# Kernel tuning notes

Measured on AMD Instinct MI355X. Metric: run time of the kernel, lower is better.

Reference implementation:

```python
import jax, jax.numpy as jnp
import numpy as np

N_NODES = 10000
N_EDGES = 640000
D_IN, D_HID, D_OUT = 128, 256, 64


def setup_inputs() -> dict:
    key = jax.random.key(0)
    k = jax.random.split(key, 8)
    h = jax.random.normal(k[0], (N_NODES, D_IN), dtype=jnp.float32)
    w = jax.random.uniform(k[1], (N_EDGES, 1), dtype=jnp.float32)
    src = jax.random.randint(k[2], (N_EDGES,), 0, N_NODES, dtype=jnp.int32)
    dst = jax.random.randint(k[3], (N_EDGES,), 0, N_NODES, dtype=jnp.int32)
    W1 = jax.random.normal(k[4], (2 * D_IN, D_HID), dtype=jnp.float32) * (1.0 / np.sqrt(2 * D_IN))
    b1 = jnp.zeros((D_HID,), dtype=jnp.float32)
    W2 = jax.random.normal(k[5], (2 * D_HID, D_OUT), dtype=jnp.float32) * (1.0 / np.sqrt(2 * D_HID))
    b2 = jnp.zeros((D_OUT,), dtype=jnp.float32)
    return {"h": h, "w": w, "src": src, "dst": dst, "W1": W1, "b1": b1, "W2": W2, "b2": b2}


def _sage_layer(h, w, src, dst, W, b, n_nodes):
    # message: m_e = h[src_e] * w_e  (scalar edge weight broadcast over features)
    m = h[src] * w  # [E, D]
    # mean scatter-reduce over incoming edges per destination node
    s = jax.ops.segment_sum(m, dst, num_segments=n_nodes)          # [N, D]
    deg = jax.ops.segment_sum(jnp.ones((dst.shape[0],), h.dtype), dst, num_segments=n_nodes)
    h_N = jnp.where(deg[:, None] > 0, s / jnp.maximum(deg, 1.0)[:, None], 0.0)
    # concat + linear
    return jnp.concatenate([h, h_N], axis=1) @ W + b


def reference(h, w, src, dst, W1, b1, W2, b2):
    n = h.shape[0]
    x = _sage_layer(h, w, src, dst, W1, b1, n)
    x = jax.nn.relu(x)
    return _sage_layer(x, w, src, dst, W2, b2, n)
```

## Files before the change

### kernel.cpp

```cpp
#include <hip/hip_runtime.h>
#include <hip/hip_fp16.h>


#define CAPS 64

typedef _Float16 f16x8 __attribute__((ext_vector_type(8)));
typedef float f32x4 __attribute__((ext_vector_type(4)));


__global__ void fill_k(const int* __restrict__ src, const int* __restrict__ dst,
                       const float* __restrict__ w, int* __restrict__ cursor,
                       unsigned int* __restrict__ ebuf, int E) {
  int i = blockIdx.x * blockDim.x + threadIdx.x;
  if (i < E) {
    const int d = dst[i];
    const int sub = i & 3;
    const int p = atomicAdd(&cursor[d * 4 + sub], 1);
    if (p < CAPS) {
      const __half hw = __float2half_rn(w[i]);
      ebuf[((size_t)(d * 4 + sub)) * CAPS + p] =
          ((unsigned int)src[i] << 16) | (unsigned int)__half_as_ushort(hw);
    }
  }
}

__global__ void cast_h_k(const float* __restrict__ h, __half* __restrict__ hh, int n4) {
  int i = blockIdx.x * blockDim.x + threadIdx.x;
  if (i < n4) {
    float4 v = reinterpret_cast<const float4*>(h)[i];
    reinterpret_cast<__half2*>(hh)[2 * i] = __floats2half2_rn(v.x, v.y);
    reinterpret_cast<__half2*>(hh)[2 * i + 1] = __floats2half2_rn(v.z, v.w);
  }
}

__global__ void w1swz_k(const float* __restrict__ W1, __half* __restrict__ Bz) {
  const int t = blockIdx.x * blockDim.x + threadIdx.x;
  if (t >= 8192) return;
  const int lane = t & 63;
  const int nt = (t >> 6) & 15;
  const int kc = t >> 10;
  const int kbase = kc * 32 + (lane >> 4) * 8;
  const int n = nt * 16 + (lane & 15);
  __half tmp[8];
#pragma unroll
  for (int j = 0; j < 8; ++j)
    tmp[j] = __float2half_rn(W1[(size_t)(kbase + j) * 256 + n]);
  *reinterpret_cast<uint4*>(Bz + (size_t)t * 8) = *reinterpret_cast<uint4*>(tmp);
}

__global__ void w2swz_k(const float* __restrict__ W2, __half* __restrict__ Bz) {
  const int t = blockIdx.x * blockDim.x + threadIdx.x;
  if (t >= 4096) return;
  const int lane = t & 63;
  const int nt = (t >> 6) & 7;
  const int kc = t >> 9;
  const int kbase = kc * 32 + (lane >> 4) * 8;
  const int np = nt * 16 + (lane & 15);
  __half tmp[8];
#pragma unroll
  for (int j = 0; j < 8; ++j) {
    const int k = kbase + j;
    const float v = (np < 64) ? W2[(size_t)k * 64 + np]
                              : W2[(size_t)(256 + k) * 64 + (np - 64)];
    tmp[j] = __float2half_rn(v);
  }
  *reinterpret_cast<uint4*>(Bz + (size_t)t * 8) = *reinterpret_cast<uint4*>(tmp);
}


__global__ __launch_bounds__(256) void agg1_k(const __half* __restrict__ hh,
                                              const unsigned int* __restrict__ ebuf,
                                              const int* __restrict__ cnt,
                                              __half* __restrict__ G1, int N) {
  const int n = blockIdx.x * 4 + (threadIdx.x >> 6);
  if (n >= N) return;
  const int lane = threadIdx.x & 63;
  const int g = lane >> 5;
  const int f = lane & 31;
  const uint2* __restrict__ H = reinterpret_cast<const uint2*>(hh);
  float a0 = 0.f, a1 = 0.f, a2 = 0.f, a3 = 0.f;
  int deg = 0;
#pragma unroll
  for (int seg = 0; seg < 4; ++seg) {
    const int m = min(cnt[n * 4 + seg], CAPS);
    deg += m;
    const unsigned int* __restrict__ bkt = ebuf + ((size_t)(n * 4 + seg)) * CAPS;
    const unsigned int pk = (lane < m) ? bkt[lane] : 0u;
    int j = 0;
    for (; j + 3 < m; j += 4) {
      const unsigned int pA = __shfl(pk, j + g);
      const unsigned int pB = __shfl(pk, j + 2 + g);
      const int eA = (int)(pA >> 16), eB = (int)(pB >> 16);
      const float wA = __half2float(__ushort_as_half((unsigned short)pA));
      const float wB = __half2float(__ushort_as_half((unsigned short)pB));
      const uint2 qA = H[(size_t)eA * 32 + f];
      const uint2 qB = H[(size_t)eB * 32 + f];
      const float2 fA0 = __half22float2(*(const __half2*)&qA.x);
      const float2 fA1 = __half22float2(*(const __half2*)&qA.y);
      const float2 fB0 = __half22float2(*(const __half2*)&qB.x);
      const float2 fB1 = __half22float2(*(const __half2*)&qB.y);
      a0 += fA0.x * wA + fB0.x * wB;
      a1 += fA0.y * wA + fB0.y * wB;
      a2 += fA1.x * wA + fB1.x * wB;
      a3 += fA1.y * wA + fB1.y * wB;
    }
    for (; j < m; j += 2) {
      const int jj = j + g;
      const unsigned int p = __shfl(pk, jj < m ? jj : (m - 1));
      const int e = (int)(p >> 16);
      float wt = __half2float(__ushort_as_half((unsigned short)p));
      if (jj >= m) wt = 0.f;
      const uint2 q = H[(size_t)e * 32 + f];
      const float2 f0 = __half22float2(*(const __half2*)&q.x);
      const float2 f1 = __half22float2(*(const __half2*)&q.y);
      a0 += f0.x * wt;
      a1 += f0.y * wt;
      a2 += f1.x * wt;
      a3 += f1.y * wt;
    }
  }
  a0 += __shfl_xor(a0, 32);
  a1 += __shfl_xor(a1, 32);
  a2 += __shfl_xor(a2, 32);
  a3 += __shfl_xor(a3, 32);
  if (lane < 32) {
    const float inv = (deg > 0) ? 1.0f / (float)deg : 0.0f;
    const __half2 p01 = __floats2half2_rn(a0 * inv, a1 * inv);
    const __half2 p23 = __floats2half2_rn(a2 * inv, a3 * inv);
    uint2 q;
    q.x = *reinterpret_cast<const unsigned int*>(&p01);
    q.y = *reinterpret_cast<const unsigned int*>(&p23);
    reinterpret_cast<uint2*>(G1)[(size_t)n * 32 + lane] = q;
  }
}


__global__ __launch_bounds__(256) void gemm1_k(const __half* __restrict__ hh,
                                               const __half* __restrict__ G1,
                                               const __half* __restrict__ Bz,
                                               const float* __restrict__ bias,
                                               __half* __restrict__ H1) {
  const int tid = threadIdx.x;
  const int w = tid >> 6, lane = tid & 63;
  const int m0 = blockIdx.x * 16;
  const int row_in = m0 + (lane & 15);
  const int qoff = (lane >> 4) * 8;
  f32x4 acc[4] = {};
  const __half* __restrict__ Ah = hh + (size_t)row_in * 128;
  const __half* __restrict__ Ag = G1 + (size_t)row_in * 128;
#pragma unroll
  for (int kc = 0; kc < 8; ++kc) {
    const __half* asrc = (kc < 4) ? (Ah + kc * 32 + qoff) : (Ag + (kc - 4) * 32 + qoff);
    const f16x8 af = *reinterpret_cast<const f16x8*>(asrc);
    const __half* bbase = Bz + ((size_t)(kc * 16 + w * 4) * 64 + lane) * 8;
#pragma unroll
    for (int nt = 0; nt < 4; ++nt) {
      const f16x8 bf = *reinterpret_cast<const f16x8*>(bbase + (size_t)nt * 64 * 8);
      acc[nt] = __builtin_amdgcn_mfma_f32_16x16x32_f16(af, bf, acc[nt], 0, 0, 0);
    }
  }
  __shared__ __half Hs[16][264];
  const int colq = lane & 15;
  const int rowq = (lane >> 4) * 4;
#pragma unroll
  for (int nt = 0; nt < 4; ++nt) {
    const int col = w * 64 + nt * 16 + colq;
    const float bz = bias[col];
#pragma unroll
    for (int r = 0; r < 4; ++r)
      Hs[rowq + r][col] = __float2half_rn(fmaxf(acc[nt][r] + bz, 0.f));
  }
  __syncthreads();
  const int r8 = tid >> 5;
  const int c32 = tid & 31;
#pragma unroll
  for (int it = 0; it < 2; ++it) {
    const int row = it * 8 + r8;
    const uint4 q = *reinterpret_cast<const uint4*>(&Hs[row][c32 * 8]);
    *reinterpret_cast<uint4*>(&H1[((size_t)(m0 + row)) * 256 + c32 * 8]) = q;
  }
}


__global__ __launch_bounds__(256) void gemmZU_k(const __half* __restrict__ H1,
                                                const __half* __restrict__ Bz,
                                                __half* __restrict__ Z,
                                                float* __restrict__ U, int M) {
  const int tid = threadIdx.x;
  const int w = tid >> 6, lane = tid & 63;
  const int m0 = blockIdx.x * 32;
  const int mh = w >> 1, nh = w & 1;
  const int row_in = m0 + mh * 16 + (lane & 15);
  const int qoff = (lane >> 4) * 8;
  f32x4 acc[4] = {};
  const __half* __restrict__ Ar = H1 + (size_t)row_in * 256;
#pragma unroll
  for (int kc = 0; kc < 8; ++kc) {
    const f16x8 af = *reinterpret_cast<const f16x8*>(Ar + kc * 32 + qoff);
    const __half* bbase = Bz + ((size_t)(kc * 8 + nh * 4) * 64 + lane) * 8;
#pragma unroll
    for (int nt = 0; nt < 4; ++nt) {
      const f16x8 bf = *reinterpret_cast<const f16x8*>(bbase + (size_t)nt * 64 * 8);
      acc[nt] = __builtin_amdgcn_mfma_f32_16x16x32_f16(af, bf, acc[nt], 0, 0, 0);
    }
  }
  __shared__ float S[32][132];
  const int colq = lane & 15;
  const int rowq = (lane >> 4) * 4;
#pragma unroll
  for (int nt = 0; nt < 4; ++nt) {
    const int col = nh * 64 + nt * 16 + colq;
#pragma unroll
    for (int r = 0; r < 4; ++r) S[mh * 16 + rowq + r][col] = acc[nt][r];
  }
  __syncthreads();
#pragma unroll
  for (int it = 0; it < 2; ++it) {
    const int idx = it * 256 + tid;
    const int row = idx >> 4, c4 = idx & 15;
    const int grow = m0 + row;
    if (grow < M) {
      const float4 v = make_float4(S[row][c4 * 4], S[row][c4 * 4 + 1],
                                   S[row][c4 * 4 + 2], S[row][c4 * 4 + 3]);
      *reinterpret_cast<float4*>(&U[(size_t)grow * 64 + c4 * 4]) = v;
    }
  }
  {
    const int row = tid >> 3, c8 = tid & 7;
    const int grow = m0 + row;
    if (grow < M) {
      const float* s = &S[row][64 + c8 * 8];
      const __half2 h0 = __floats2half2_rn(s[0], s[1]);
      const __half2 h1 = __floats2half2_rn(s[2], s[3]);
      const __half2 h2 = __floats2half2_rn(s[4], s[5]);
      const __half2 h3 = __floats2half2_rn(s[6], s[7]);
      uint4 q;
      q.x = *reinterpret_cast<const unsigned int*>(&h0);
      q.y = *reinterpret_cast<const unsigned int*>(&h1);
      q.z = *reinterpret_cast<const unsigned int*>(&h2);
      q.w = *reinterpret_cast<const unsigned int*>(&h3);
      *reinterpret_cast<uint4*>(&Z[(size_t)grow * 64 + c8 * 8]) = q;
    }
  }
}


__global__ __launch_bounds__(256) void agg2z_k(const __half* __restrict__ Z,
                                               const float* __restrict__ U,
                                               const float* __restrict__ b2,
                                               const unsigned int* __restrict__ ebuf,
                                               const int* __restrict__ cnt,
                                               float* __restrict__ out, int N) {
  const int n = blockIdx.x * 4 + (threadIdx.x >> 6);
  if (n >= N) return;
  const int lane = threadIdx.x & 63;
  const int g = lane >> 4;
  const int f = lane & 15;
  const uint2* __restrict__ Zr = reinterpret_cast<const uint2*>(Z);
  float a0 = 0.f, a1 = 0.f, a2 = 0.f, a3 = 0.f;
  int deg = 0;
#pragma unroll
  for (int seg = 0; seg < 4; ++seg) {
    const int m = min(cnt[n * 4 + seg], CAPS);
    deg += m;
    const unsigned int* __restrict__ bkt = ebuf + ((size_t)(n * 4 + seg)) * CAPS;
    const unsigned int pk = (lane < m) ? bkt[lane] : 0u;
    int j = 0;
    for (; j + 7 < m; j += 8) {
      const unsigned int pA = __shfl(pk, j + g);
      const unsigned int pB = __shfl(pk, j + 4 + g);
      const int eA = (int)(pA >> 16), eB = (int)(pB >> 16);
      const float wA = __half2float(__ushort_as_half((unsigned short)pA));
      const float wB = __half2float(__ushort_as_half((unsigned short)pB));
      const uint2 qA = Zr[(size_t)eA * 16 + f];
      const uint2 qB = Zr[(size_t)eB * 16 + f];
      const float2 fA0 = __half22float2(*(const __half2*)&qA.x);
      const float2 fA1 = __half22float2(*(const __half2*)&qA.y);
      const float2 fB0 = __half22float2(*(const __half2*)&qB.x);
      const float2 fB1 = __half22float2(*(const __half2*)&qB.y);
      a0 += fA0.x * wA + fB0.x * wB;
      a1 += fA0.y * wA + fB0.y * wB;
      a2 += fA1.x * wA + fB1.x * wB;
      a3 += fA1.y * wA + fB1.y * wB;
    }
    for (; j < m; j += 4) {
      const int jj = j + g;
      const unsigned int p = __shfl(pk, jj < m ? jj : (m - 1));
      const int e = (int)(p >> 16);
      float wt = __half2float(__ushort_as_half((unsigned short)p));
      if (jj >= m) wt = 0.f;
      const uint2 q = Zr[(size_t)e * 16 + f];
      const float2 f0 = __half22float2(*(const __half2*)&q.x);
      const float2 f1 = __half22float2(*(const __half2*)&q.y);
      a0 += f0.x * wt;
      a1 += f0.y * wt;
      a2 += f1.x * wt;
      a3 += f1.y * wt;
    }
  }
  a0 += __shfl_xor(a0, 16); a1 += __shfl_xor(a1, 16);
  a2 += __shfl_xor(a2, 16); a3 += __shfl_xor(a3, 16);
  a0 += __shfl_xor(a0, 32); a1 += __shfl_xor(a1, 32);
  a2 += __shfl_xor(a2, 32); a3 += __shfl_xor(a3, 32);
  if (lane < 16) {
    const float inv = (deg > 0) ? 1.0f / (float)deg : 0.0f;
    const float4 u = *reinterpret_cast<const float4*>(&U[(size_t)n * 64 + 4 * f]);
    const float4 bz = *reinterpret_cast<const float4*>(&b2[4 * f]);
    float4 o;
    o.x = a0 * inv + u.x + bz.x;
    o.y = a1 * inv + u.y + bz.y;
    o.z = a2 * inv + u.z + bz.z;
    o.w = a3 * inv + u.w + bz.w;
    *reinterpret_cast<float4*>(&out[(size_t)n * 64 + 4 * f]) = o;
  }
}


extern "C" void kernel_launch(void* const* d_in, const int* in_sizes, int n_in,
                              void* d_out, int out_size, void* d_ws, size_t ws_size,
                              hipStream_t stream) {
  const float* h   = (const float*)d_in[0];
  const float* w   = (const float*)d_in[1];
  const int*   src = (const int*)d_in[2];
  const int*   dst = (const int*)d_in[3];
  const float* W1  = (const float*)d_in[4];
  const float* b1  = (const float*)d_in[5];
  const float* W2  = (const float*)d_in[6];
  const float* b2  = (const float*)d_in[7];
  float* out = (float*)d_out;

  const int N = in_sizes[0] / 128;
  const int E = in_sizes[2];
  const int Mpad = ((N + 31) / 32) * 32;

  char* ws = (char*)d_ws;
  size_t o = 0;
  auto alloc = [&](size_t bytes) -> void* {
    void* p = ws + o;
    o = (o + bytes + 255) & ~(size_t)255;
    return p;
  };
  int*          cursor = (int*)alloc((size_t)N * 4 * 4);
  unsigned int* ebuf   = (unsigned int*)alloc((size_t)N * 4 * CAPS * 4);
  __half*       hh     = (__half*)alloc((size_t)N * 128 * 2);
  __half*       G1     = (__half*)alloc((size_t)N * 128 * 2);
  __half*       H1     = (__half*)alloc((size_t)Mpad * 256 * 2);
  __half*       Z      = (__half*)alloc((size_t)Mpad * 64 * 2);
  float*        U      = (float*)alloc((size_t)Mpad * 64 * 4);
  __half*       W1z    = (__half*)alloc((size_t)256 * 256 * 2);
  __half*       W2z    = (__half*)alloc((size_t)256 * 128 * 2);

  hipMemsetAsync(cursor, 0, (size_t)N * 4 * 4, stream);
  fill_k<<<(E + 255) / 256, 256, 0, stream>>>(src, dst, w, cursor, ebuf, E);
  cast_h_k<<<(N * 128 / 4 + 255) / 256, 256, 0, stream>>>(h, hh, N * 128 / 4);
  w1swz_k<<<32, 256, 0, stream>>>(W1, W1z);
  w2swz_k<<<16, 256, 0, stream>>>(W2, W2z);

  agg1_k<<<(N + 3) / 4, 256, 0, stream>>>(hh, ebuf, cursor, G1, N);

  gemm1_k<<<N / 16, 256, 0, stream>>>(hh, G1, W1z, b1, H1);

  gemmZU_k<<<(N + 31) / 32, 256, 0, stream>>>(H1, W2z, Z, U, N);

  agg2z_k<<<(N + 3) / 4, 256, 0, stream>>>(Z, U, b2, ebuf, cursor, out, N);
}
```

Measured before the change: 160.1 us.

## Fuse prep kernels, fuse the two GEMMs, and split edge buckets into eight sub-bins

Merges the memset, h cast and both weight swizzles into one prep kernel, cutting launch count. Fuses the layer-1 GEMM with the layer-2 Z/U projection, so the hidden activations stay in shared memory instead of round-tripping through a global H1 buffer. Also raises the edge sub-buckets from 4 to 8 with capacity 32 each, which spreads atomic contention in fill_k but adds more per-node segment loop iterations in the aggregation kernels. The per-bucket capacity drop raises the risk of dropping edges at skewed degrees.

Measured after the change: 166.0 us. 3.7% more time.

```diff
diff --git a/kernel.cpp b/kernel.cpp
--- a/kernel.cpp
+++ b/kernel.cpp
@@ -2,10 +2,65 @@
 #include <hip/hip_fp16.h>
 
 
-#define CAPS 64
+#define NSUB 8
+#define CAPS 32
 
 typedef _Float16 f16x8 __attribute__((ext_vector_type(8)));
 typedef float f32x4 __attribute__((ext_vector_type(4)));
+
+
+__global__ __launch_bounds__(256) void prep_k(const float* __restrict__ h,
+                                              const float* __restrict__ W1,
+                                              const float* __restrict__ W2,
+                                              int* __restrict__ cursor,
+                                              __half* __restrict__ hh,
+                                              __half* __restrict__ W1z,
+                                              __half* __restrict__ W2z,
+                                              int NC, int NH4) {
+  const int t = blockIdx.x * blockDim.x + threadIdx.x;
+  if (t < NC) {
+    cursor[t] = 0;
+    return;
+  }
+  const int tc = t - NC;
+  if (tc < NH4) {
+    const float4 v = reinterpret_cast<const float4*>(h)[tc];
+    reinterpret_cast<__half2*>(hh)[2 * tc] = __floats2half2_rn(v.x, v.y);
+    reinterpret_cast<__half2*>(hh)[2 * tc + 1] = __floats2half2_rn(v.z, v.w);
+    return;
+  }
+  const int tw1 = tc - NH4;
+  if (tw1 < 8192) {
+    const int lane = tw1 & 63;
+    const int nt = (tw1 >> 6) & 15;
+    const int kc = tw1 >> 10;
+    const int kbase = kc * 32 + (lane >> 4) * 8;
+    const int n = nt * 16 + (lane & 15);
+    __half tmp[8];
+#pragma unroll
+    for (int j = 0; j < 8; ++j)
+      tmp[j] = __float2half_rn(W1[(size_t)(kbase + j) * 256 + n]);
+    *reinterpret_cast<uint4*>(W1z + (size_t)tw1 * 8) = *reinterpret_cast<uint4*>(tmp);
+    return;
+  }
+  const int tw2 = tw1 - 8192;
+  if (tw2 < 4096) {
+    const int lane = tw2 & 63;
+    const int nt = (tw2 >> 6) & 7;
+    const int kc = tw2 >> 9;
+    const int kbase = kc * 32 + (lane >> 4) * 8;
+    const int np = nt * 16 + (lane & 15);
+    __half tmp[8];
+#pragma unroll
+    for (int j = 0; j < 8; ++j) {
+      const int k = kbase + j;
+      const float v = (np < 64) ? W2[(size_t)k * 64 + np]
+                                : W2[(size_t)(256 + k) * 64 + (np - 64)];
+      tmp[j] = __float2half_rn(v);
+    }
+    *reinterpret_cast<uint4*>(W2z + (size_t)tw2 * 8) = *reinterpret_cast<uint4*>(tmp);
+  }
+}
 
 
 __global__ void fill_k(const int* __restrict__ src, const int* __restrict__ dst,
@@ -14,57 +69,14 @@
   int i = blockIdx.x * blockDim.x + threadIdx.x;
   if (i < E) {
     const int d = dst[i];
-    const int sub = i & 3;
-    const int p = atomicAdd(&cursor[d * 4 + sub], 1);
+    const int sub = i & (NSUB - 1);
+    const int p = atomicAdd(&cursor[d * NSUB + sub], 1);
     if (p < CAPS) {
       const __half hw = __float2half_rn(w[i]);
-      ebuf[((size_t)(d * 4 + sub)) * CAPS + p] =
+      ebuf[((size_t)(d * NSUB + sub)) * CAPS + p] =
           ((unsigned int)src[i] << 16) | (unsigned int)__half_as_ushort(hw);
     }
   }
-}
-
-__global__ void cast_h_k(const float* __restrict__ h, __half* __restrict__ hh, int n4) {
-  int i = blockIdx.x * blockDim.x + threadIdx.x;
-  if (i < n4) {
-    float4 v = reinterpret_cast<const float4*>(h)[i];
-    reinterpret_cast<__half2*>(hh)[2 * i] = __floats2half2_rn(v.x, v.y);
-    reinterpret_cast<__half2*>(hh)[2 * i + 1] = __floats2half2_rn(v.z, v.w);
-  }
-}
-
-__global__ void w1swz_k(const float* __restrict__ W1, __half* __restrict__ Bz) {
-  const int t = blockIdx.x * blockDim.x + threadIdx.x;
-  if (t >= 8192) return;
-  const int lane = t & 63;
-  const int nt = (t >> 6) & 15;
-  const int kc = t >> 10;
-  const int kbase = kc * 32 + (lane >> 4) * 8;
-  const int n = nt * 16 + (lane & 15);
-  __half tmp[8];
-#pragma unroll
-  for (int j = 0; j < 8; ++j)
-    tmp[j] = __float2half_rn(W1[(size_t)(kbase + j) * 256 + n]);
-  *reinterpret_cast<uint4*>(Bz + (size_t)t * 8) = *reinterpret_cast<uint4*>(tmp);
-}
-
-__global__ void w2swz_k(const float* __restrict__ W2, __half* __restrict__ Bz) {
-  const int t = blockIdx.x * blockDim.x + threadIdx.x;
-  if (t >= 4096) return;
-  const int lane = t & 63;
-  const int nt = (t >> 6) & 7;
-  const int kc = t >> 9;
-  const int kbase = kc * 32 + (lane >> 4) * 8;
-  const int np = nt * 16 + (lane & 15);
-  __half tmp[8];
-#pragma unroll
-  for (int j = 0; j < 8; ++j) {
-    const int k = kbase + j;
-    const float v = (np < 64) ? W2[(size_t)k * 64 + np]
-                              : W2[(size_t)(256 + k) * 64 + (np - 64)];
-    tmp[j] = __float2half_rn(v);
-  }
-  *reinterpret_cast<uint4*>(Bz + (size_t)t * 8) = *reinterpret_cast<uint4*>(tmp);
 }
 
 
@@ -80,11 +92,10 @@
   const uint2* __restrict__ H = reinterpret_cast<const uint2*>(hh);
   float a0 = 0.f, a1 = 0.f, a2 = 0.f, a3 = 0.f;
   int deg = 0;
-#pragma unroll
-  for (int seg = 0; seg < 4; ++seg) {
-    const int m = min(cnt[n * 4 + seg], CAPS);
+  for (int seg = 0; seg < NSUB; ++seg) {
+    const int m = min(cnt[n * NSUB + seg], CAPS);
     deg += m;
-    const unsigned int* __restrict__ bkt = ebuf + ((size_t)(n * 4 + seg)) * CAPS;
+    const unsigned int* __restrict__ bkt = ebuf + ((size_t)(n * NSUB + seg)) * CAPS;
     const unsigned int pk = (lane < m) ? bkt[lane] : 0u;
     int j = 0;
     for (; j + 3 < m; j += 4) {
@@ -135,16 +146,21 @@
 }
 
 
-__global__ __launch_bounds__(256) void gemm1_k(const __half* __restrict__ hh,
-                                               const __half* __restrict__ G1,
-                                               const __half* __restrict__ Bz,
-                                               const float* __restrict__ bias,
-                                               __half* __restrict__ H1) {
+__global__ __launch_bounds__(256) void gemm1zu_k(const __half* __restrict__ hh,
+                                                 const __half* __restrict__ G1,
+                                                 const __half* __restrict__ W1z,
+                                                 const float* __restrict__ b1,
+                                                 const __half* __restrict__ W2z,
+                                                 __half* __restrict__ Z,
+                                                 float* __restrict__ U) {
   const int tid = threadIdx.x;
   const int w = tid >> 6, lane = tid & 63;
   const int m0 = blockIdx.x * 16;
   const int row_in = m0 + (lane & 15);
   const int qoff = (lane >> 4) * 8;
+  const int colq = lane & 15;
+  const int rowq = (lane >> 4) * 4;
+
   f32x4 acc[4] = {};
   const __half* __restrict__ Ah = hh + (size_t)row_in * 128;
   const __half* __restrict__ Ag = G1 + (size_t)row_in * 128;
@@ -152,95 +168,62 @@
   for (int kc = 0; kc < 8; ++kc) {
     const __half* asrc = (kc < 4) ? (Ah + kc * 32 + qoff) : (Ag + (kc - 4) * 32 + qoff);
     const f16x8 af = *reinterpret_cast<const f16x8*>(asrc);
-    const __half* bbase = Bz + ((size_t)(kc * 16 + w * 4) * 64 + lane) * 8;
+    const __half* bbase = W1z + ((size_t)(kc * 16 + w * 4) * 64 + lane) * 8;
 #pragma unroll
     for (int nt = 0; nt < 4; ++nt) {
       const f16x8 bf = *reinterpret_cast<const f16x8*>(bbase + (size_t)nt * 64 * 8);
       acc[nt] = __builtin_amdgcn_mfma_f32_16x16x32_f16(af, bf, acc[nt], 0, 0, 0);
     }
   }
-  __shared__ __half Hs[16][264];
-  const int colq = lane & 15;
-  const int rowq = (lane >> 4) * 4;
+  __shared__ alignas(16) __half Hs[16][264];
 #pragma unroll
   for (int nt = 0; nt < 4; ++nt) {
     const int col = w * 64 + nt * 16 + colq;
-    const float bz = bias[col];
+    const float bz = b1[col];
 #pragma unroll
     for (int r = 0; r < 4; ++r)
       Hs[rowq + r][col] = __float2half_rn(fmaxf(acc[nt][r] + bz, 0.f));
   }
   __syncthreads();
-  const int r8 = tid >> 5;
-  const int c32 = tid & 31;
-#pragma unroll
-  for (int it = 0; it < 2; ++it) {
-    const int row = it * 8 + r8;
-    const uint4 q = *reinterpret_cast<const uint4*>(&Hs[row][c32 * 8]);
-    *reinterpret_cast<uint4*>(&H1[((size_t)(m0 + row)) * 256 + c32 * 8]) = q;
-  }
-}
-
-
-__global__ __launch_bounds__(256) void gemmZU_k(const __half* __restrict__ H1,
-                                                const __half* __restrict__ Bz,
-                                                __half* __restrict__ Z,
-                                                float* __restrict__ U, int M) {
-  const int tid = threadIdx.x;
-  const int w = tid >> 6, lane = tid & 63;
-  const int m0 = blockIdx.x * 32;
-  const int mh = w >> 1, nh = w & 1;
-  const int row_in = m0 + mh * 16 + (lane & 15);
-  const int qoff = (lane >> 4) * 8;
-  f32x4 acc[4] = {};
-  const __half* __restrict__ Ar = H1 + (size_t)row_in * 256;
+
+  f32x4 accz[2] = {};
 #pragma unroll
   for (int kc = 0; kc < 8; ++kc) {
-    const f16x8 af = *reinterpret_cast<const f16x8*>(Ar + kc * 32 + qoff);
-    const __half* bbase = Bz + ((size_t)(kc * 8 + nh * 4) * 64 + lane) * 8;
-#pragma unroll
-    for (int nt = 0; nt < 4; ++nt) {
+    const f16x8 af = *reinterpret_cast<const f16x8*>(&Hs[lane & 15][kc * 32 + qoff]);
+    const __half* bbase = W2z + ((size_t)(kc * 8 + w * 2) * 64 + lane) * 8;
+#pragma unroll
+    for (int nt = 0; nt < 2; ++nt) {
       const f16x8 bf = *reinterpret_cast<const f16x8*>(bbase + (size_t)nt * 64 * 8);
-      acc[nt] = __builtin_amdgcn_mfma_f32_16x16x32_f16(af, bf, acc[nt], 0, 0, 0);
-    }
-  }
-  __shared__ float S[32][132];
-  const int colq = lane & 15;
-  const int rowq = (lane >> 4) * 4;
-#pragma unroll
-  for (int nt = 0; nt < 4; ++nt) {
-    const int col = nh * 64 + nt * 16 + colq;
-#pragma unroll
-    for (int r = 0; r < 4; ++r) S[mh * 16 + rowq + r][col] = acc[nt][r];
+      accz[nt] = __builtin_amdgcn_mfma_f32_16x16x32_f16(af, bf, accz[nt], 0, 0, 0);
+    }
+  }
+  __shared__ float S[16][132];
+#pragma unroll
+  for (int nt = 0; nt < 2; ++nt) {
+    const int col = w * 32 + nt * 16 + colq;
+#pragma unroll
+    for (int r = 0; r < 4; ++r) S[rowq + r][col] = accz[nt][r];
   }
   __syncthreads();
-#pragma unroll
-  for (int it = 0; it < 2; ++it) {
-    const int idx = it * 256 + tid;
-    const int row = idx >> 4, c4 = idx & 15;
-    const int grow = m0 + row;
-    if (grow < M) {
-      const float4 v = make_float4(S[row][c4 * 4], S[row][c4 * 4 + 1],
-                                   S[row][c4 * 4 + 2], S[row][c4 * 4 + 3]);
-      *reinterpret_cast<float4*>(&U[(size_t)grow * 64 + c4 * 4]) = v;
-    }
-  }
   {
+    const int row = tid >> 4, c4 = tid & 15;
+    const float4 v = make_float4(S[row][c4 * 4], S[row][c4 * 4 + 1],
+                                 S[row][c4 * 4 + 2], S[row][c4 * 4 + 3]);
+    *reinterpret_cast<float4*>(&U[(size_t)(m0 + row) * 64 + c4 * 4]) = v;
+  }
+  if (tid < 128) {
     const int row = tid >> 3, c8 = tid & 7;
-    const int grow = m0 + row;
-    if (grow < M) {
-      const float* s = &S[row][64 + c8 * 8];
-      const __half2 h0 = __floats2half2_rn(s[0], s[1]);
-      const __half2 h1 = __floats2half2_rn(s[2], s[3]);
-      const __half2 h2 = __floats2half2_rn(s[4], s[5]);
-      const __half2 h3 = __floats2half2_rn(s[6], s[7]);
-      uint4 q;
-      q.x = *reinterpret_cast<const unsigned int*>(&h0);
-      q.y = *reinterpret_cast<const unsigned int*>(&h1);
-      q.z = *reinterpret_cast<const unsigned int*>(&h2);
-      q.w = *reinterpret_cast<const unsigned int*>(&h3);
-      *reinterpret_cast<uint4*>(&Z[(size_t)grow * 64 + c8 * 8]) = q;
-    }
+    const float* s = &S[row][64 + c8 * 8];
+    const __half2 h0 = __floats2half2_rn(s[0], s[1]);
+    const __half2 h1 = __floats2half2_rn(s[2], s[3]);
+    const __half2 h2 = __floats2half2_rn(s[4], s[5]);
+    const __half2 h3 = __floats2half2_rn(s[6], s[7]);
+    uint4 q;
+    q.x = *reinterpret_cast<const unsigned int*>(&h0);
+    q.y = *reinterpret_cast<const unsigned int*>(&h1);
+    q.z = *reinterpret_cast<const unsigned int*>(&h2);
+    q.w = *reinterpret_cast<const unsigned int*>(&h3);
+    *reinterpret_cast<uint4*>(&Z[(size_t)(m0 + row) * 64 + c8 * 8]) = q;
   }
 }
 
@@ -259,11 +242,10 @@
   const uint2* __restrict__ Zr = reinterpret_cast<const uint2*>(Z);
   float a0 = 0.f, a1 = 0.f, a2 = 0.f, a3 = 0.f;
   int deg = 0;
-#pragma unroll
-  for (int seg = 0; seg < 4; ++seg) {
-    const int m = min(cnt[n * 4 + seg], CAPS);
+  for (int seg = 0; seg < NSUB; ++seg) {
+    const int m = min(cnt[n * NSUB + seg], CAPS);
     deg += m;
-    const unsigned int* __restrict__ bkt = ebuf + ((size_t)(n * 4 + seg)) * CAPS;
+    const unsigned int* __restrict__ bkt = ebuf + ((size_t)(n * NSUB + seg)) * CAPS;
     const unsigned int pk = (lane < m) ? bkt[lane] : 0u;
     int j = 0;
     for (; j + 7 < m; j += 8) {
@@ -331,7 +313,6 @@
 
   const int N = in_sizes[0] / 128;
   const int E = in_sizes[2];
-  const int Mpad = ((N + 31) / 32) * 32;
 
   char* ws = (char*)d_ws;
   size_t o = 0;
@@ -340,27 +321,22 @@
     o = (o + bytes + 255) & ~(size_t)255;
     return p;
   };
-  int*          cursor = (int*)alloc((size_t)N * 4 * 4);
-  unsigned int* ebuf   = (unsigned int*)alloc((size_t)N * 4 * CAPS * 4);
+  int*          cursor = (int*)alloc((size_t)N * NSUB * 4);
+  unsigned int* ebuf   = (unsigned int*)alloc((size_t)N * NSUB * CAPS * 4);
   __half*       hh     = (__half*)alloc((size_t)N * 128 * 2);
   __half*       G1     = (__half*)alloc((size_t)N * 128 * 2);
-  __half*       H1     = (__half*)alloc((size_t)Mpad * 256 * 2);
-  __half*       Z      = (__half*)alloc((size_t)Mpad * 64 * 2);
-  float*        U      = (float*)alloc((size_t)Mpad * 64 * 4);
+  __half*       Z      = (__half*)alloc((size_t)N * 64 * 2);
+  float*        U      = (float*)alloc((size_t)N * 64 * 4);
   __half*       W1z    = (__half*)alloc((size_t)256 * 256 * 2);
   __half*       W2z    = (__half*)alloc((size_t)256 * 128 * 2);
 
-  hipMemsetAsync(cursor, 0, (size_t)N * 4 * 4, stream);
+  const int NC = N * NSUB;
+  const int NH4 = N * 128 / 4;
+  const int prep_threads = NC + NH4 + 8192 + 4096;
+  prep_k<<<(prep_threads + 255) / 256, 256, 0, stream>>>(h, W1, W2, cursor, hh,
+                                                         W1z, W2z, NC, NH4);
   fill_k<<<(E + 255) / 256, 256, 0, stream>>>(src, dst, w, cursor, ebuf, E);
-  cast_h_k<<<(N * 128 / 4 + 255) / 256, 256, 0, stream>>>(h, hh, N * 128 / 4);
-  w1swz_k<<<32, 256, 0, stream>>>(W1, W1z);
-  w2swz_k<<<16, 256, 0, stream>>>(W2, W2z);
-
   agg1_k<<<(N + 3) / 4, 256, 0, stream>>>(hh, ebuf, cursor, G1, N);
-
-  gemm1_k<<<N / 16, 256, 0, stream>>>(hh, G1, W1z, b1, H1);
-
-  gemmZU_k<<<(N + 31) / 32, 256, 0, stream>>>(H1, W2z, Z, U, N);
-
+  gemm1zu_k<<<N / 16, 256, 0, stream>>>(hh, G1, W1z, b1, W2z, Z, U);
   agg2z_k<<<(N + 3) / 4, 256, 0, stream>>>(Z, U, b2, ebuf, cursor, out, N);
 }
```
